# Optimization experiments

Measured on AMD Instinct MI355X. Metric: run time of the kernel, lower is better.

Reference implementation:

```python
import jax, jax.numpy as jnp
import numpy as np

B, C, H, W = 128, 768, 14, 14
D = 128          # d_graph
K = 8            # top_k
LN_EPS = 1e-5
NORM_EPS = 1e-12


def setup_inputs() -> dict:
    key = jax.random.key(0)
    ks = jax.random.split(key, 12)
    s = lambda k, shape, fan: jax.random.normal(k, shape, jnp.float32) / np.sqrt(fan)
    return {
        "feat_map": jax.random.normal(ks[0], (B, C, H, W), jnp.float32),
        # node_proj: Linear(C, D) + LayerNorm(D)
        "W_node": s(ks[1], (C, D), C), "b_node": jnp.zeros((D,), jnp.float32),
        "ln_g": jnp.ones((D,), jnp.float32), "ln_b": jnp.zeros((D,), jnp.float32),
        # pos_mlp: Linear(2, 64) -> GELU -> Linear(64, D)
        "Wp1": s(ks[2], (2, 64), 2), "bp1": jnp.zeros((64,), jnp.float32),
        "Wp2": s(ks[3], (64, D), 64), "bp2": jnp.zeros((D,), jnp.float32),
        # edge_mlp: Linear(3D, D) -> GELU -> Linear(D, D)
        "We1": s(ks[4], (3 * D, D), 3 * D), "be1": jnp.zeros((D,), jnp.float32),
        "We2": s(ks[5], (D, D), D), "be2": jnp.zeros((D,), jnp.float32),
    }


def _layernorm(x, g, b):
    mu = jnp.mean(x, axis=-1, keepdims=True)
    var = jnp.mean(jnp.square(x - mu), axis=-1, keepdims=True)
    return (x - mu) * jax.lax.rsqrt(var + LN_EPS) * g + b


def reference(feat_map, W_node, b_node, ln_g, ln_b, Wp1, bp1, Wp2, bp2, We1, be1, We2, be2):
    Bm, Cm, Hm, Wm = feat_map.shape
    N = Hm * Wm
    tokens = feat_map.reshape(Bm, Cm, N).transpose(0, 2, 1)            # [B,N,C]
    nodes = jax.nn.gelu(_layernorm(tokens @ W_node + b_node, ln_g, ln_b), approximate=False)  # [B,N,D]

    ys = jnp.linspace(0.0, 1.0, Hm)
    xs = jnp.linspace(0.0, 1.0, Wm)
    gy, gx = jnp.meshgrid(ys, xs, indexing='ij')
    coords = jnp.stack([gy.reshape(-1), gx.reshape(-1)], axis=-1)       # [N,2]
    coords = jnp.broadcast_to(coords[None], (Bm, N, 2))

    nrm = nodes / jnp.maximum(jnp.linalg.norm(nodes, axis=-1, keepdims=True), NORM_EPS)
    sim = jnp.einsum('bnd,bmd->bnm', nrm, nrm)
    sim = sim - jnp.eye(N, dtype=sim.dtype)[None] * 1e9
    _, adj = jax.lax.top_k(sim, K)                                      # [B,N,K]

    adj_flat = adj.reshape(Bm, N * K, 1)
    neighbor_nodes = jnp.take_along_axis(nodes, adj_flat, axis=1).reshape(Bm, N, K, -1)
    neighbor_coords = jnp.take_along_axis(coords, adj_flat, axis=1).reshape(Bm, N, K, 2)

    disp = neighbor_coords - coords[:, :, None, :]                      # [B,N,K,2]
    spatial_feat = jax.nn.gelu(disp @ Wp1 + bp1, approximate=False) @ Wp2 + bp2  # [B,N,K,D]

    source = jnp.broadcast_to(nodes[:, :, None, :], neighbor_nodes.shape)
    edge_input = jnp.concatenate([source, neighbor_nodes, spatial_feat], axis=-1)  # [B,N,K,3D]
    edges = jax.nn.gelu(edge_input @ We1 + be1, approximate=False) @ We2 + be2
    return nodes, edges, adj
```

## Files before the change

### kernel.cpp

```cpp
#include <hip/hip_runtime.h>

#define BB 128
#define CC 768
#define NN 196
#define DD 128
#define KTOP 8
#define MROWS 25088

typedef unsigned short u16;
typedef unsigned int u32;

typedef __attribute__((ext_vector_type(8))) short bf16x8;
typedef __attribute__((ext_vector_type(4))) float f32x4;

__device__ __forceinline__ u16 f2bfu(float x) {
    u32 i; __builtin_memcpy(&i, &x, 4);
    u32 r = (i + 0x7fffu + ((i >> 16) & 1u)) >> 16;
    return (u16)r;
}
__device__ __forceinline__ float gelu_f(float x) {
    return 0.5f * x * (1.0f + erff(x * 0.70710678118654752f));
}

__global__ __launch_bounds__(256)
void gemm_node_kernel(const float* __restrict__ feat, const float* __restrict__ Wn,
                      float* __restrict__ part)
{
    __shared__ float As[32][64];
    __shared__ float Bs[32][DD];
    const int tid = threadIdx.x;
    const int m0  = blockIdx.x * 64;
    const int k0  = blockIdx.y * 384;

    const int r_ld   = tid & 63;
    const int cl_ld  = tid >> 6;
    const int m_ld   = m0 + r_ld;
    const int b_ld   = m_ld / NN;
    const int n_ld   = m_ld % NN;
    const float* fbase = feat + (size_t)b_ld * CC * NN + n_ld;

    const int rg = tid >> 5;
    const int cg = tid & 31;

    float acc[8][4];
#pragma unroll
    for (int i = 0; i < 8; ++i)
#pragma unroll
        for (int j = 0; j < 4; ++j) acc[i][j] = 0.0f;

    for (int kt = 0; kt < 12; ++kt) {
        const int kbase = k0 + kt * 32;
#pragma unroll
        for (int p = 0; p < 8; ++p) {
            const int cl = cl_ld + 4 * p;
            As[cl][r_ld] = fbase[(size_t)(kbase + cl) * NN];
        }
#pragma unroll
        for (int p = 0; p < 4; ++p) {
            const int q = tid + 256 * p;
            const int cl = q >> 5, d4 = (q & 31) * 4;
            *(float4*)(&Bs[cl][d4]) = *(const float4*)(&Wn[(size_t)(kbase + cl) * DD + d4]);
        }
        __syncthreads();
#pragma unroll
        for (int kk = 0; kk < 32; ++kk) {
            const float4 a0 = *(const float4*)(&As[kk][rg * 8]);
            const float4 a1 = *(const float4*)(&As[kk][rg * 8 + 4]);
            const float4 bv = *(const float4*)(&Bs[kk][cg * 4]);
            const float af[8] = {a0.x, a0.y, a0.z, a0.w, a1.x, a1.y, a1.z, a1.w};
#pragma unroll
            for (int i = 0; i < 8; ++i) {
                acc[i][0] += af[i] * bv.x; acc[i][1] += af[i] * bv.y;
                acc[i][2] += af[i] * bv.z; acc[i][3] += af[i] * bv.w;
            }
        }
        __syncthreads();
    }
    float* op = part + ((size_t)blockIdx.y * MROWS + m0 + rg * 8) * DD + cg * 4;
#pragma unroll
    for (int i = 0; i < 8; ++i) {
        *(float4*)(op + (size_t)i * DD) =
            make_float4(acc[i][0], acc[i][1], acc[i][2], acc[i][3]);
    }
}

__global__ __launch_bounds__(128)
void ln_kernel(const float* __restrict__ part, const float* __restrict__ bnode,
               const float* __restrict__ lng, const float* __restrict__ lnb,
               float* __restrict__ nodes, float* __restrict__ inv_norm)
{
    __shared__ float vals[8][DD];
    __shared__ float stats[8][2];
    const int tid = threadIdx.x;
    const int row0 = blockIdx.x * 8;
    const int d = tid;
    const float bb = bnode[d];
#pragma unroll
    for (int r = 0; r < 8; ++r) {
        const size_t m = row0 + r;
        vals[r][d] = part[m * DD + d] + part[(size_t)(MROWS + m) * DD + d] + bb;
    }
    __syncthreads();
    const int lane = tid & 63, wv = tid >> 6;
    for (int r = wv * 4; r < wv * 4 + 4; ++r) {
        float a0 = vals[r][lane], a1 = vals[r][lane + 64];
        float s = a0 + a1;
#pragma unroll
        for (int off = 32; off > 0; off >>= 1) s += __shfl_xor(s, off);
        const float mu = s * (1.0f / 128.0f);
        float d0 = a0 - mu, d1 = a1 - mu;
        float s2 = d0 * d0 + d1 * d1;
#pragma unroll
        for (int off = 32; off > 0; off >>= 1) s2 += __shfl_xor(s2, off);
        if (lane == 0) { stats[r][0] = mu; stats[r][1] = rsqrtf(s2 * (1.0f/128.0f) + 1e-5f); }
    }
    __syncthreads();
    const float g  = lng[d];
    const float be = lnb[d];
    float acc[8];
#pragma unroll
    for (int r = 0; r < 8; ++r) {
        const float y = (vals[r][d] - stats[r][0]) * stats[r][1] * g + be;
        acc[r] = gelu_f(y);
    }
    __syncthreads();
#pragma unroll
    for (int r = 0; r < 8; ++r) vals[r][d] = acc[r] * acc[r];
#pragma unroll
    for (int r = 0; r < 8; ++r) nodes[(size_t)(row0 + r) * DD + d] = acc[r];
    __syncthreads();
    for (int r = wv * 4; r < wv * 4 + 4; ++r) {
        float s = vals[r][lane] + vals[r][lane + 64];
#pragma unroll
        for (int off = 32; off > 0; off >>= 1) s += __shfl_xor(s, off);
        if (lane == 0) inv_norm[row0 + r] = 1.0f / fmaxf(sqrtf(s), 1e-12f);
    }
}

__global__ __launch_bounds__(256)
void s1n1_kernel(const float* __restrict__ nodes, const float* __restrict__ We1,
                 float* __restrict__ S1, float* __restrict__ N1)
{
    __shared__ float atile[64][DD];
    const int tid = threadIdx.x;
    const int row0 = blockIdx.x * 64;
#pragma unroll
    for (int p = 0; p < 8; ++p) {
        const int idx = tid + 256 * p;
        const int r = idx >> 5, q = idx & 31;
        *(float4*)(&atile[r][q * 4]) = *(const float4*)(&nodes[(size_t)(row0 + r) * DD + q * 4]);
    }
    __syncthreads();
    const int rg = tid >> 5;
    const int cg = tid & 31;
    const int r0 = rg * 8;
    const int c0 = cg * 8;
    const float* wbase = (c0 < DD) ? (We1 + c0) : (We1 + 128 * DD + (c0 - DD));
    float acc[8][8];
#pragma unroll
    for (int i = 0; i < 8; ++i)
#pragma unroll
        for (int j = 0; j < 8; ++j) acc[i][j] = 0.0f;
    for (int k = 0; k < DD; k += 4) {
        float4 av[8];
#pragma unroll
        for (int ri = 0; ri < 8; ++ri) av[ri] = *(const float4*)(&atile[r0 + ri][k]);
#pragma unroll
        for (int kk = 0; kk < 4; ++kk) {
            const float4 w0 = *(const float4*)(wbase + (size_t)(k + kk) * DD);
            const float4 w1 = *(const float4*)(wbase + (size_t)(k + kk) * DD + 4);
            const float wf[8] = {w0.x, w0.y, w0.z, w0.w, w1.x, w1.y, w1.z, w1.w};
#pragma unroll
            for (int ri = 0; ri < 8; ++ri) {
                const float a = (kk == 0) ? av[ri].x : (kk == 1) ? av[ri].y : (kk == 2) ? av[ri].z : av[ri].w;
#pragma unroll
                for (int ci = 0; ci < 8; ++ci) acc[ri][ci] += a * wf[ci];
            }
        }
    }
    float* outp = (c0 < DD) ? (S1 + (size_t)row0 * DD + c0)
                            : (N1 + (size_t)row0 * DD + (c0 - DD));
#pragma unroll
    for (int ri = 0; ri < 8; ++ri) {
        *(float4*)(outp + (size_t)(r0 + ri) * DD) =
            make_float4(acc[ri][0], acc[ri][1], acc[ri][2], acc[ri][3]);
        *(float4*)(outp + (size_t)(r0 + ri) * DD + 4) =
            make_float4(acc[ri][4], acc[ri][5], acc[ri][6], acc[ri][7]);
    }
}

__global__ __launch_bounds__(256)
void sim_kernel(const float* __restrict__ nodes, const float* __restrict__ inv_norm,
                float* __restrict__ sim)
{
    __shared__ float as[28][36];
    __shared__ float bs[NN][36];
    __shared__ float invs[NN];
    const int tid = threadIdx.x;
    const int b  = blockIdx.x / 7;
    const int n0 = (blockIdx.x % 7) * 28;
    const float* nb = nodes + (size_t)b * NN * DD;
    if (tid < NN) invs[tid] = inv_norm[b * NN + tid];
    const bool act = tid < 196;
    const int ai = act ? tid / 28 : 0;
    const int bi = act ? tid % 28 : 0;
    float acc[4][7];
#pragma unroll
    for (int r = 0; r < 4; ++r)
#pragma unroll
        for (int j = 0; j < 7; ++j) acc[r][j] = 0.0f;
    for (int dc = 0; dc < DD; dc += 32) {
        __syncthreads();
        if (tid < 224) {
            const int i = tid >> 3, q = tid & 7;
            *(float4*)(&as[i][q * 4]) = *(const float4*)(&nb[(size_t)(n0 + i) * DD + dc + q * 4]);
        }
        for (int idx = tid; idx < 1568; idx += 256) {
            const int r = idx >> 3, q = idx & 7;
            *(float4*)(&bs[r][q * 4]) = *(const float4*)(&nb[(size_t)r * DD + dc + q * 4]);
        }
        __syncthreads();
        if (act) {
            for (int dd = 0; dd < 32; dd += 4) {
                float4 a4[4], b4[7];
#pragma unroll
                for (int r = 0; r < 4; ++r) a4[r] = *(const float4*)(&as[ai * 4 + r][dd]);
#pragma unroll
                for (int j = 0; j < 7; ++j) b4[j] = *(const float4*)(&bs[bi * 7 + j][dd]);
#pragma unroll
                for (int r = 0; r < 4; ++r)
#pragma unroll
                    for (int j = 0; j < 7; ++j)
                        acc[r][j] += a4[r].x * b4[j].x + a4[r].y * b4[j].y
                                   + a4[r].z * b4[j].z + a4[r].w * b4[j].w;
            }
        }
    }
    if (act) {
#pragma unroll
        for (int r = 0; r < 4; ++r) {
            const int n = n0 + ai * 4 + r;
            const float sn = invs[n];
#pragma unroll
            for (int j = 0; j < 7; ++j) {
                const int m = bi * 7 + j;
                sim[((size_t)b * NN + n) * NN + m] = acc[r][j] * sn * invs[m];
            }
        }
    }
}

__global__ __launch_bounds__(64)
void topk_kernel(const float* __restrict__ sim, int* __restrict__ adj_i,
                 float* __restrict__ adj_o, const float* __restrict__ We2,
                 uint4* __restrict__ W2P)
{
    const int bn = blockIdx.x;
    if (bn >= BB * NN) {
        const int e  = (bn - BB * NN) * 64 + threadIdx.x;
        const int l  = e & 63;
        const int fi = e >> 6;
        const int ks = fi >> 3, ct = fi & 7;
        const int k0 = ks * 32 + (l >> 4) * 8;
        const int c  = ct * 16 + (l & 15);
        u16 v[8];
#pragma unroll
        for (int j = 0; j < 8; ++j) v[j] = f2bfu(We2[(size_t)(k0 + j) * DD + c]);
        uint4 pk;
        pk.x = (u32)v[0] | ((u32)v[1] << 16);
        pk.y = (u32)v[2] | ((u32)v[3] << 16);
        pk.z = (u32)v[4] | ((u32)v[5] << 16);
        pk.w = (u32)v[6] | ((u32)v[7] << 16);
        W2P[e] = pk;
        return;
    }
    const int n = bn % NN;
    const int lane = threadIdx.x;
    const float* srow = sim + (size_t)bn * NN;
    float v[4]; int mi[4];
#pragma unroll
    for (int s = 0; s < 4; ++s) {
        const int m = lane + 64 * s;
        mi[s] = m;
        v[s] = (m < NN && m != n) ? srow[m] : -3.0e38f;
    }
    for (int r = 0; r < KTOP; ++r) {
        float bv = v[0]; int bm = mi[0];
#pragma unroll
        for (int s = 1; s < 4; ++s) { if (v[s] > bv) { bv = v[s]; bm = mi[s]; } }
#pragma unroll
        for (int off = 32; off > 0; off >>= 1) {
            const float ov = __shfl_xor(bv, off);
            const int   om = __shfl_xor(bm, off);
            if (ov > bv || (ov == bv && om < bm)) { bv = ov; bm = om; }
        }
        if (lane == 0) {
            adj_i[bn * KTOP + r] = bm;
            adj_o[bn * KTOP + r] = (float)bm;
        }
#pragma unroll
        for (int s = 0; s < 4; ++s) if (mi[s] == bm) v[s] = -3.0e38f;
    }
}

__global__ __launch_bounds__(128)
void pos_kernel(const float* __restrict__ Wp1, const float* __restrict__ bp1,
                const float* __restrict__ Wp2, const float* __restrict__ bp2,
                const float* __restrict__ We1, float* __restrict__ PC)
{
    __shared__ float t1[64];
    __shared__ float sp[DD];
    const int e = blockIdx.x;
    const int dy = e / 27 - 13, dx = e % 27 - 13;
    const float fy = (float)dy / 13.0f, fx = (float)dx / 13.0f;
    const int tid = threadIdx.x;
    if (tid < 64) {
        const float h = fy * Wp1[tid] + fx * Wp1[64 + tid] + bp1[tid];
        t1[tid] = gelu_f(h);
    }
    __syncthreads();
    float s = bp2[tid];
    for (int j = 0; j < 64; ++j) s += t1[j] * Wp2[j * DD + tid];
    sp[tid] = s;
    __syncthreads();
    float o = 0.0f;
    for (int c = 0; c < DD; ++c) o += sp[c] * We1[(size_t)(256 + c) * DD + tid];
    PC[e * DD + tid] = o;
}

__global__ __launch_bounds__(256)
void edge_kernel(const float* __restrict__ S1, const float* __restrict__ N1,
                 const float* __restrict__ PC, const int* __restrict__ adj_i,
                 const float* __restrict__ be1, const uint4* __restrict__ W2P,
                 const float* __restrict__ be2, float* __restrict__ edges_o)
{
    __shared__ uint4 ldsB[2048];
    const int tid = threadIdx.x;
    const int b  = blockIdx.x / 25;
    const int n0 = (blockIdx.x % 25) * 8;

#pragma unroll
    for (int p = 0; p < 8; ++p)
        ldsB[tid + 256 * p] = W2P[tid + 256 * p];

    const int l  = tid & 63;
    const int wv = tid >> 6;
    const int g  = l >> 4;
    const int rA = wv * 16 + (l & 15);
    const int nA0 = n0 + (rA >> 3);
    const int nA  = (nA0 < NN) ? nA0 : 0;
    const int kA  = rA & 7;
    const int m   = adj_i[((size_t)b * NN + nA) * KTOP + kA];
    const int iy = nA / 14, ix = nA % 14;
    const int my = m / 14,  mx = m % 14;
    const int di = (my - iy + 13) * 27 + (mx - ix + 13);

    const float* s1r = S1 + ((size_t)b * NN + nA) * DD;
    const float* n1r = N1 + ((size_t)b * NN + m) * DD;
    const float* pcr = PC + (size_t)di * DD;

    bf16x8 afr[4];
#pragma unroll
    for (int ks = 0; ks < 4; ++ks) {
        const int k0 = ks * 32 + g * 8;
        float u[8];
#pragma unroll
        for (int h = 0; h < 2; ++h) {
            const int k = k0 + h * 4;
            const float4 s1 = *(const float4*)(s1r + k);
            const float4 n1 = *(const float4*)(n1r + k);
            const float4 pc = *(const float4*)(pcr + k);
            const float4 b1 = *(const float4*)(be1 + k);
            u[h * 4 + 0] = gelu_f(s1.x + n1.x + pc.x + b1.x);
            u[h * 4 + 1] = gelu_f(s1.y + n1.y + pc.y + b1.y);
            u[h * 4 + 2] = gelu_f(s1.z + n1.z + pc.z + b1.z);
            u[h * 4 + 3] = gelu_f(s1.w + n1.w + pc.w + b1.w);
        }
        bf16x8 a;
#pragma unroll
        for (int j = 0; j < 8; ++j) a[j] = (short)f2bfu(u[j]);
        afr[ks] = a;
    }
    __syncthreads();

    f32x4 acc[8];
#pragma unroll
    for (int ct = 0; ct < 8; ++ct) {
        f32x4 z = {0.0f, 0.0f, 0.0f, 0.0f};
        acc[ct] = z;
    }
#pragma unroll
    for (int ks = 0; ks < 4; ++ks) {
#pragma unroll
        for (int ct = 0; ct < 8; ++ct) {
            const uint4 bw = ldsB[(ks * 8 + ct) * 64 + l];
            bf16x8 bf; __builtin_memcpy(&bf, &bw, 16);
            acc[ct] = __builtin_amdgcn_mfma_f32_16x16x32_bf16(afr[ks], bf, acc[ct], 0, 0, 0);
        }
    }

    const int cl  = l & 15;
    const int rq0 = (l >> 4) * 4;
    float be2f[8];
#pragma unroll
    for (int ct = 0; ct < 8; ++ct) be2f[ct] = be2[ct * 16 + cl];
#pragma unroll
    for (int q = 0; q < 4; ++q) {
        const int r = wv * 16 + rq0 + q;
        const int n = n0 + (r >> 3);
        if (n < NN) {
            float* op = edges_o + (((size_t)b * NN + n) * KTOP + (r & 7)) * DD;
#pragma unroll
            for (int ct = 0; ct < 8; ++ct)
                op[ct * 16 + cl] = acc[ct][q] + be2f[ct];
        }
    }
}

extern "C" void kernel_launch(void* const* d_in, const int* in_sizes, int n_in,
                              void* d_out, int out_size, void* d_ws, size_t ws_size,
                              hipStream_t stream)
{
    const float* feat = (const float*)d_in[0];
    const float* Wn   = (const float*)d_in[1];
    const float* bn   = (const float*)d_in[2];
    const float* lng  = (const float*)d_in[3];
    const float* lnb  = (const float*)d_in[4];
    const float* Wp1  = (const float*)d_in[5];
    const float* bp1  = (const float*)d_in[6];
    const float* Wp2  = (const float*)d_in[7];
    const float* bp2  = (const float*)d_in[8];
    const float* We1  = (const float*)d_in[9];
    const float* be1  = (const float*)d_in[10];
    const float* We2  = (const float*)d_in[11];
    const float* be2  = (const float*)d_in[12];

    float* ws = (float*)d_ws;
    float* part     = ws;
    float* sim      = ws;
    float* S1       = ws + 4917248;
    float* N1       = ws + 8128512;
    float* PC       = ws + 11339776;
    float* inv_norm = ws + 11433088;
    int*   adj_i    = (int*)(ws + 11458176);
    uint4* W2P      = (uint4*)(ws + 11433088);

    float* out      = (float*)d_out;
    float* nodes    = out;
    float* edges_o  = out + 3211264;
    float* adj_o    = out + 3211264 + 25690112;

    gemm_node_kernel<<<dim3(392, 2), 256, 0, stream>>>(feat, Wn, part);
    ln_kernel<<<3136, 128, 0, stream>>>(part, bn, lng, lnb, nodes, inv_norm);
    s1n1_kernel<<<392, 256, 0, stream>>>(nodes, We1, S1, N1);
    pos_kernel<<<729, 128, 0, stream>>>(Wp1, bp1, Wp2, bp2, We1, PC);
    sim_kernel<<<BB * 7, 256, 0, stream>>>(nodes, inv_norm, sim);
    topk_kernel<<<BB * NN + 32, 64, 0, stream>>>(sim, adj_i, adj_o, We2, W2P);
    edge_kernel<<<BB * 25, 256, 0, stream>>>(S1, N1, PC, adj_i, be1, W2P, be2, edges_o);
}
```

Baseline: 405.7 us.

## Use split-bf16 MFMA for S1/N1 projection and pack four top-k rows per block

Replaces the fp32 FMA GEMM in s1n1_kernel with bf16 MFMA instructions. It uses a hi/lo split (three MFMAs per tile) to keep near-fp32 accuracy, with We1 pre-packed into MFMA fragment layout by a new small kernel. Separately, topk_kernel now processes four rows per 256-thread block instead of one row per 64-thread block, which reduces block count and launch overhead. The packed weights reuse the PC workspace region before pos_kernel writes it, so ordering matters. The lower-precision split could also change results slightly.

```diff
diff --git a/kernel.cpp b/kernel.cpp
--- a/kernel.cpp
+++ b/kernel.cpp
@@ -18,8 +18,38 @@
     u32 r = (i + 0x7fffu + ((i >> 16) & 1u)) >> 16;
     return (u16)r;
 }
+__device__ __forceinline__ float bfu2f(u16 h) {
+    u32 x = ((u32)h) << 16; float f; __builtin_memcpy(&f, &x, 4); return f;
+}
+__device__ __forceinline__ void unpack2(u32 u, float& f0, float& f1) {
+    u32 lo = u << 16, hi = u & 0xffff0000u;
+    __builtin_memcpy(&f0, &lo, 4); __builtin_memcpy(&f1, &hi, 4);
+}
 __device__ __forceinline__ float gelu_f(float x) {
     return 0.5f * x * (1.0f + erff(x * 0.70710678118654752f));
+}
+
+__global__ __launch_bounds__(256)
+void pack_we1_kernel(const float* __restrict__ We1, uint4* __restrict__ WPH,
+                     uint4* __restrict__ WPL)
+{
+    const int eid = blockIdx.x * 256 + threadIdx.x;
+    const int mat = eid >> 11, rem = eid & 2047;
+    const int kc = rem >> 9, ct = (rem >> 6) & 7, l = rem & 63;
+    const int g = l >> 4, c = ct * 16 + (l & 15);
+    const int krow = mat * 128 + kc * 32 + g * 8;
+    u32 h[4], lo[4];
+#pragma unroll
+    for (int jp = 0; jp < 4; ++jp) {
+        const float w0 = We1[(size_t)(krow + 2 * jp) * DD + c];
+        const float w1 = We1[(size_t)(krow + 2 * jp + 1) * DD + c];
+        const u16 h0 = f2bfu(w0), h1 = f2bfu(w1);
+        const u16 l0 = f2bfu(w0 - bfu2f(h0)), l1 = f2bfu(w1 - bfu2f(h1));
+        h[jp]  = (u32)h0 | ((u32)h1 << 16);
+        lo[jp] = (u32)l0 | ((u32)l1 << 16);
+    }
+    WPH[eid] = make_uint4(h[0], h[1], h[2], h[3]);
+    WPL[eid] = make_uint4(lo[0], lo[1], lo[2], lo[3]);
 }
 
 __global__ __launch_bounds__(256)
@@ -138,55 +168,86 @@
 }
 
 __global__ __launch_bounds__(256)
-void s1n1_kernel(const float* __restrict__ nodes, const float* __restrict__ We1,
-                 float* __restrict__ S1, float* __restrict__ N1)
-{
-    __shared__ float atile[64][DD];
+void s1n1_kernel(const float* __restrict__ nodes, const uint4* __restrict__ WPH,
+                 const uint4* __restrict__ WPL, float* __restrict__ S1,
+                 float* __restrict__ N1)
+{
+    __shared__ uint4 AfH[4][4][64];
+    __shared__ uint4 AfL[4][4][64];
     const int tid = threadIdx.x;
-    const int row0 = blockIdx.x * 64;
+    const int m0 = blockIdx.x * 64;
+
 #pragma unroll
     for (int p = 0; p < 8; ++p) {
         const int idx = tid + 256 * p;
-        const int r = idx >> 5, q = idx & 31;
-        *(float4*)(&atile[r][q * 4]) = *(const float4*)(&nodes[(size_t)(row0 + r) * DD + q * 4]);
-    }
-    __syncthreads();
-    const int rg = tid >> 5;
-    const int cg = tid & 31;
-    const int r0 = rg * 8;
-    const int c0 = cg * 8;
-    const float* wbase = (c0 < DD) ? (We1 + c0) : (We1 + 128 * DD + (c0 - DD));
-    float acc[8][8];
-#pragma unroll
-    for (int i = 0; i < 8; ++i)
-#pragma unroll
-        for (int j = 0; j < 8; ++j) acc[i][j] = 0.0f;
-    for (int k = 0; k < DD; k += 4) {
-        float4 av[8];
-#pragma unroll
-        for (int ri = 0; ri < 8; ++ri) av[ri] = *(const float4*)(&atile[r0 + ri][k]);
-#pragma unroll
-        for (int kk = 0; kk < 4; ++kk) {
-            const float4 w0 = *(const float4*)(wbase + (size_t)(k + kk) * DD);
-            const float4 w1 = *(const float4*)(wbase + (size_t)(k + kk) * DD + 4);
-            const float wf[8] = {w0.x, w0.y, w0.z, w0.w, w1.x, w1.y, w1.z, w1.w};
-#pragma unroll
-            for (int ri = 0; ri < 8; ++ri) {
-                const float a = (kk == 0) ? av[ri].x : (kk == 1) ? av[ri].y : (kk == 2) ? av[ri].z : av[ri].w;
-#pragma unroll
-                for (int ci = 0; ci < 8; ++ci) acc[ri][ci] += a * wf[ci];
+        const int r = idx >> 5, d0 = (idx & 31) * 4;
+        const float4 v = *(const float4*)(&nodes[(size_t)(m0 + r) * DD + d0]);
+        const u16 h0 = f2bfu(v.x), h1 = f2bfu(v.y), h2 = f2bfu(v.z), h3 = f2bfu(v.w);
+        const u16 l0 = f2bfu(v.x - bfu2f(h0)), l1 = f2bfu(v.y - bfu2f(h1));
+        const u16 l2 = f2bfu(v.z - bfu2f(h2)), l3 = f2bfu(v.w - bfu2f(h3));
+        const int rt = r >> 4, kc = d0 >> 5;
+        const int ln = (((d0 >> 3) & 3) << 4) | (r & 15);
+        const int half = (d0 >> 2) & 1;
+        u32* ph = (u32*)&AfH[rt][kc][ln];
+        u32* pl = (u32*)&AfL[rt][kc][ln];
+        ph[half * 2]     = (u32)h0 | ((u32)h1 << 16);
+        ph[half * 2 + 1] = (u32)h2 | ((u32)h3 << 16);
+        pl[half * 2]     = (u32)l0 | ((u32)l1 << 16);
+        pl[half * 2 + 1] = (u32)l2 | ((u32)l3 << 16);
+    }
+    __syncthreads();
+
+    const int l  = tid & 63;
+    const int wv = tid >> 6;
+    const int wr = wv >> 1, wc = wv & 1;
+
+    f32x4 acc[2][8];
+#pragma unroll
+    for (int rt = 0; rt < 2; ++rt)
+#pragma unroll
+        for (int ct = 0; ct < 8; ++ct) {
+            f32x4 z = {0.0f, 0.0f, 0.0f, 0.0f};
+            acc[rt][ct] = z;
+        }
+
+#pragma unroll
+    for (int kc = 0; kc < 4; ++kc) {
+        bf16x8 aH[2], aL[2];
+#pragma unroll
+        for (int rt = 0; rt < 2; ++rt) {
+            const uint4 uh = AfH[wr * 2 + rt][kc][l];
+            const uint4 ul = AfL[wr * 2 + rt][kc][l];
+            __builtin_memcpy(&aH[rt], &uh, 16);
+            __builtin_memcpy(&aL[rt], &ul, 16);
+        }
+#pragma unroll
+        for (int ct = 0; ct < 8; ++ct) {
+            const uint4 uh = WPH[((wc * 4 + kc) * 8 + ct) * 64 + l];
+            const uint4 ul = WPL[((wc * 4 + kc) * 8 + ct) * 64 + l];
+            bf16x8 bH, bL;
+            __builtin_memcpy(&bH, &uh, 16);
+            __builtin_memcpy(&bL, &ul, 16);
+#pragma unroll
+            for (int rt = 0; rt < 2; ++rt) {
+                acc[rt][ct] = __builtin_amdgcn_mfma_f32_16x16x32_bf16(aH[rt], bH, acc[rt][ct], 0, 0, 0);
+                acc[rt][ct] = __builtin_amdgcn_mfma_f32_16x16x32_bf16(aL[rt], bH, acc[rt][ct], 0, 0, 0);
+                acc[rt][ct] = __builtin_amdgcn_mfma_f32_16x16x32_bf16(aH[rt], bL, acc[rt][ct], 0, 0, 0);
             }
         }
     }
-    float* outp = (c0 < DD) ? (S1 + (size_t)row0 * DD + c0)
-                            : (N1 + (size_t)row0 * DD + (c0 - DD));
-#pragma unroll
-    for (int ri = 0; ri < 8; ++ri) {
-        *(float4*)(outp + (size_t)(r0 + ri) * DD) =
-            make_float4(acc[ri][0], acc[ri][1], acc[ri][2], acc[ri][3]);
-        *(float4*)(outp + (size_t)(r0 + ri) * DD + 4) =
-            make_float4(acc[ri][4], acc[ri][5], acc[ri][6], acc[ri][7]);
-    }
+
+    float* outb = wc ? N1 : S1;
+    const int cl  = l & 15;
+    const int rq0 = (l >> 4) * 4;
+#pragma unroll
+    for (int rt = 0; rt < 2; ++rt)
+#pragma unroll
+        for (int q = 0; q < 4; ++q) {
+            const size_t row = m0 + wr * 32 + rt * 16 + rq0 + q;
+#pragma unroll
+            for (int ct = 0; ct < 8; ++ct)
+                outb[row * DD + ct * 16 + cl] = acc[rt][ct][q];
+        }
 }
 
 __global__ __launch_bounds__(256)
@@ -250,14 +311,14 @@
     }
 }
 
-__global__ __launch_bounds__(64)
+__global__ __launch_bounds__(256)
 void topk_kernel(const float* __restrict__ sim, int* __restrict__ adj_i,
                  float* __restrict__ adj_o, const float* __restrict__ We2,
                  uint4* __restrict__ W2P)
 {
-    const int bn = blockIdx.x;
-    if (bn >= BB * NN) {
-        const int e  = (bn - BB * NN) * 64 + threadIdx.x;
+    const int bid = blockIdx.x;
+    if (bid >= (BB * NN) / 4) {
+        const int e  = (bid - (BB * NN) / 4) * 256 + threadIdx.x;
         const int l  = e & 63;
         const int fi = e >> 6;
         const int ks = fi >> 3, ct = fi & 7;
@@ -274,8 +335,9 @@
         W2P[e] = pk;
         return;
     }
+    const int bn = bid * 4 + (threadIdx.x >> 6);
     const int n = bn % NN;
-    const int lane = threadIdx.x;
+    const int lane = threadIdx.x & 63;
     const float* srow = sim + (size_t)bn * NN;
     float v[4]; int mi[4];
 #pragma unroll
@@ -444,17 +506,20 @@
     float* inv_norm = ws + 11433088;
     int*   adj_i    = (int*)(ws + 11458176);
     uint4* W2P      = (uint4*)(ws + 11433088);
+    uint4* WPH      = (uint4*)(ws + 11339776);
+    uint4* WPL      = WPH + 4096;
 
     float* out      = (float*)d_out;
     float* nodes    = out;
     float* edges_o  = out + 3211264;
     float* adj_o    = out + 3211264 + 25690112;
 
+    pack_we1_kernel<<<16, 256, 0, stream>>>(We1, WPH, WPL);
     gemm_node_kernel<<<dim3(392, 2), 256, 0, stream>>>(feat, Wn, part);
     ln_kernel<<<3136, 128, 0, stream>>>(part, bn, lng, lnb, nodes, inv_norm);
-    s1n1_kernel<<<392, 256, 0, stream>>>(nodes, We1, S1, N1);
+    s1n1_kernel<<<392, 256, 0, stream>>>(nodes, WPH, WPL, S1, N1);
     pos_kernel<<<729, 128, 0, stream>>>(Wp1, bp1, Wp2, bp2, We1, PC);
     sim_kernel<<<BB * 7, 256, 0, stream>>>(nodes, inv_norm, sim);
-    topk_kernel<<<BB * NN + 32, 64, 0, stream>>>(sim, adj_i, adj_o, We2, W2P);
+    topk_kernel<<<(BB * NN) / 4 + 8, 256, 0, stream>>>(sim, adj_i, adj_o, We2, W2P);
     edge_kernel<<<BB * 25, 256, 0, stream>>>(S1, N1, PC, adj_i, be1, W2P, be2, edges_o);
 }
```

Result: no change. 404.3 us (-0.3%).
